# Performance work log

Measured on AMD Instinct MI355X. Metric: run time of the kernel, lower is better.

## Reference

```python
import jax, jax.numpy as jnp
import numpy as np

M, N = 1024, 4096


def setup_inputs() -> dict:
    key = jax.random.key(0)
    k1, k2, k3 = jax.random.split(key, 3)
    scores = jax.random.normal(k1, (M, N), dtype=jnp.float32)
    continuing_ag = jax.random.randint(k2, (M,), 0, 2).astype(jnp.int32)
    joint_action_prev = jax.random.randint(k3, (M,), 0, N).astype(jnp.int32)
    return {"scores": scores, "continuing_ag": continuing_ag,
            "joint_action_prev": joint_action_prev}


def _assign(policy, continuing_ag, joint_action_prev):
    """Sequential greedy bipartite assignment (train=False / argmax path)."""
    m, n = policy.shape
    cont = continuing_ag.astype(bool)
    # Pre-assign continuing agents and zero their rows and chosen columns.
    out0 = jnp.where(cont, joint_action_prev, jnp.full((m,), -1, jnp.int32))
    col_hit = (jnp.zeros((n,), jnp.float32)
               .at[joint_action_prev].add(continuing_ag.astype(jnp.float32))) > 0
    pol0 = policy * (~cont)[:, None].astype(policy.dtype) * (~col_hit)[None, :].astype(policy.dtype)
    rows = jnp.arange(m)
    cols = jnp.arange(n)

    def step(carry, i):
        pol, act = carry
        flat = pol.reshape(-1)
        idx = jnp.argmax(flat)
        # skip if this agent is continuing, or all entries already zeroed
        do = (~cont[i]) & jnp.any(flat > 0)
        a = idx // n
        t = (idx % n).astype(act.dtype)
        act = act.at[a].set(jnp.where(do, t, act[a]))
        keep = ~((rows == a)[:, None] | (cols == (idx % n))[None, :])
        pol = jnp.where(do, pol * keep.astype(pol.dtype), pol)
        return (pol, act), None

    (_, act), _ = jax.lax.scan(step, (pol0, out0), jnp.arange(m))
    return act


def reference(scores, continuing_ag, joint_action_prev):
    # get_policy: softmax over the flattened M*N score matrix
    policy = jax.nn.softmax(scores.reshape(-1)).reshape(scores.shape)
    actions = _assign(policy, continuing_ag, joint_action_prev)
    return actions, policy
```

## Files before the change

### kernel.cpp

```cpp
#include <hip/hip_runtime.h>
#include <cstdint>
#include <cstddef>

#define MROWS 1024
#define NCOLS 4096
#define KCAP 12

typedef unsigned long long u64;
typedef unsigned int u32;

__device__ inline u32 fkey(u32 b) { return (b & 0x80000000u) ? ~b : (b | 0x80000000u); }

__device__ inline int key_col(u64 k) { return (NCOLS - 1) - (int)(k & 0xFFFull); }
__device__ inline int key_row(u64 k) { return (MROWS - 1) - (int)((k >> 12) & 0x3FFull); }

#define WAVE_FENCE() __asm__ volatile("s_waitcnt lgkmcnt(0)" ::: "memory")

__device__ inline float wave_sum_f(float v) {
    #pragma unroll
    for (int off = 32; off >= 1; off >>= 1)
        v += __shfl_xor(v, off, 64);
    return v;
}
__device__ inline u64 wave_max_u64(u64 v) {
    #pragma unroll
    for (int off = 32; off >= 1; off >>= 1) {
        u64 o = __shfl_xor(v, off, 64);
        v = o > v ? o : v;
    }
    return v;
}
__device__ inline u64 umax64(u64 a, u64 b) { return a > b ? a : b; }

__global__ __launch_bounds__(256, 4) void k_prep(const float* __restrict__ s,
                                                 float* __restrict__ rowsum,
                                                 u64* __restrict__ keys_g) {
    __shared__ u64 list[4][KCAP];
    __shared__ u32 cnts[4];
    int w = threadIdx.x >> 6, lane = threadIdx.x & 63;
    int r = blockIdx.x * 4 + w;

    const float4* s4 = (const float4*)(s + (size_t)r * NCOLS);
    u64 rowpart = (u64)(MROWS - 1 - r) << 12;
    if (lane == 0) cnts[w] = 0u;
    WAVE_FENCE();

    float acc = 0.0f;
    #pragma unroll
    for (int j = 0; j < 16; ++j) {
        float4 v = s4[lane + j * 64];
        acc += __expf(v.x) + __expf(v.y) + __expf(v.z) + __expf(v.w);
        int c0 = 4 * (lane + j * 64);
        if (v.x > 2.85f) { u32 sl = atomicAdd(&cnts[w], 1u); if (sl < KCAP)
            list[w][sl] = ((u64)fkey(__float_as_uint(v.x)) << 22) | rowpart | (u64)(NCOLS - 1 - (c0 + 0)); }
        if (v.y > 2.85f) { u32 sl = atomicAdd(&cnts[w], 1u); if (sl < KCAP)
            list[w][sl] = ((u64)fkey(__float_as_uint(v.y)) << 22) | rowpart | (u64)(NCOLS - 1 - (c0 + 1)); }
        if (v.z > 2.85f) { u32 sl = atomicAdd(&cnts[w], 1u); if (sl < KCAP)
            list[w][sl] = ((u64)fkey(__float_as_uint(v.z)) << 22) | rowpart | (u64)(NCOLS - 1 - (c0 + 2)); }
        if (v.w > 2.85f) { u32 sl = atomicAdd(&cnts[w], 1u); if (sl < KCAP)
            list[w][sl] = ((u64)fkey(__float_as_uint(v.w)) << 22) | rowpart | (u64)(NCOLS - 1 - (c0 + 3)); }
    }
    acc = wave_sum_f(acc);
    if (lane == 0) rowsum[r] = acc;
    WAVE_FENCE();
    u32 n = cnts[w];

    for (int att = 1; att < 4; ++att) {
        if (n <= KCAP) break;
        float T = att == 1 ? 3.1f : att == 2 ? 3.4f : 3.8f;
        if (lane == 0) cnts[w] = 0u;
        WAVE_FENCE();
        #pragma unroll 4
        for (int j = 0; j < 16; ++j) {
            float4 v = s4[lane + j * 64];
            int c0 = 4 * (lane + j * 64);
            if (v.x > T) { u32 sl = atomicAdd(&cnts[w], 1u); if (sl < KCAP)
                list[w][sl] = ((u64)fkey(__float_as_uint(v.x)) << 22) | rowpart | (u64)(NCOLS - 1 - (c0 + 0)); }
            if (v.y > T) { u32 sl = atomicAdd(&cnts[w], 1u); if (sl < KCAP)
                list[w][sl] = ((u64)fkey(__float_as_uint(v.y)) << 22) | rowpart | (u64)(NCOLS - 1 - (c0 + 1)); }
            if (v.z > T) { u32 sl = atomicAdd(&cnts[w], 1u); if (sl < KCAP)
                list[w][sl] = ((u64)fkey(__float_as_uint(v.z)) << 22) | rowpart | (u64)(NCOLS - 1 - (c0 + 2)); }
            if (v.w > T) { u32 sl = atomicAdd(&cnts[w], 1u); if (sl < KCAP)
                list[w][sl] = ((u64)fkey(__float_as_uint(v.w)) << 22) | rowpart | (u64)(NCOLS - 1 - (c0 + 3)); }
        }
        WAVE_FENCE();
        n = cnts[w];
    }
    if (n > KCAP) n = 0;
    if (lane < KCAP)
        keys_g[(size_t)r * KCAP + lane] = (lane < n) ? list[w][lane] : 0ull;
}

__global__ __launch_bounds__(512, 1) void k_policy_match(const float* __restrict__ s,
                                                         const int* __restrict__ cont,
                                                         const int* __restrict__ prev,
                                                         const float* __restrict__ rowsum,
                                                         const u64* __restrict__ keys_g,
                                                         float* __restrict__ policy,
                                                         float* __restrict__ actions) {
    __shared__ u64 keybuf[MROWS * KCAP];
    __shared__ u64 colbest[NCOLS];
    __shared__ u64 cand[64];
    __shared__ u32 coldone[NCOLS / 32];
    __shared__ u32 rowdone[MROWS / 32];
    __shared__ float act[MROWS];
    __shared__ u32 leftrows[64];
    __shared__ int nleft;
    __shared__ float fredf[8];

    int t = threadIdx.x;
    int wid = t >> 6, lane = t & 63;

    if (blockIdx.x != 0) {
        int r = blockIdx.x - 1;
        const float4* srow4 = (const float4*)(s + (size_t)r * NCOLS);
        float4 v0 = srow4[t], v1 = srow4[t + 512];
        float sv = rowsum[t] + rowsum[t + 512];
        sv = wave_sum_f(sv);
        if (lane == 0) fredf[wid] = sv;
        __syncthreads();
        float g = 0.0f;
        #pragma unroll
        for (int i = 0; i < 8; ++i) g += fredf[i];
        float inv = 1.0f / g;
        float4* prow4 = (float4*)(policy + (size_t)r * NCOLS);
        float4 p;
        p.x = __expf(v0.x) * inv; p.y = __expf(v0.y) * inv;
        p.z = __expf(v0.z) * inv; p.w = __expf(v0.w) * inv;
        prow4[t] = p;
        p.x = __expf(v1.x) * inv; p.y = __expf(v1.y) * inv;
        p.z = __expf(v1.z) * inv; p.w = __expf(v1.w) * inv;
        prow4[t + 512] = p;
        return;
    }

    {
        const float4* kg4 = (const float4*)keys_g;
        float4* kb4 = (float4*)keybuf;
        #pragma unroll
        for (int i = 0; i < 12; ++i) kb4[t + i * 512] = kg4[t + i * 512];
        #pragma unroll
        for (int i = 0; i < 8; ++i) colbest[t + i * 512] = 0ull;
        if (t < 128) coldone[t] = 0u;
        if (t < 64) cand[t] = 0ull;
        if (t < 32) rowdone[t] = 0u;
        if (t == 0) nleft = 0;
    }
    __syncthreads();

    int r0 = t, r1 = t + 512;
    int c0f = cont[r0], c1f = cont[r1];
    int p0 = prev[r0], p1 = prev[r1];
    act[r0] = c0f ? (float)p0 : -1.0f;
    act[r1] = c1f ? (float)p1 : -1.0f;
    if (c0f) {
        atomicOr(&rowdone[r0 >> 5], 1u << (r0 & 31));
        atomicOr(&coldone[p0 >> 5], 1u << (p0 & 31));
    }
    if (c1f) {
        atomicOr(&rowdone[r1 >> 5], 1u << (r1 & 31));
        atomicOr(&coldone[p1 >> 5], 1u << (p1 & 31));
    }
    bool act0 = (c0f == 0), act1 = (c1f == 0);

    const u64* kb0 = keybuf + (size_t)r0 * KCAP;
    const u64* kb1 = keybuf + (size_t)r1 * KCAP;
    u32 m0 = 0u, m1 = 0u;
    #pragma unroll
    for (int k = 0; k < KCAP; ++k) {
        if (kb0[k] != 0ull) m0 |= 1u << k;
        if (kb1[k] != 0ull) m1 |= 1u << k;
    }
    if (m0 == 0u) act0 = false;
    if (m1 == 0u) act1 = false;
    __syncthreads();

    for (int round = 1; round < 500; ++round) {
        u64 tag = (u64)round << 54;
        bool sub0 = false, sub1 = false;
        u64 best0 = 0ull, best1 = 0ull;
        if (act0) {
            u32 m = m0;
            #pragma unroll
            for (int k = 0; k < KCAP; ++k) {
                if (m & (1u << k)) {
                    u64 kk = kb0[k];
                    int c = key_col(kk);
                    if ((coldone[c >> 5] >> (c & 31)) & 1u) m &= ~(1u << k);
                    else {
                        best0 = umax64(best0, kk);
                        atomicMax((u64*)&colbest[c], tag | kk);
                    }
                }
            }
            m0 = m;
            if (best0 == 0ull) act0 = false;
            else sub0 = true;
        }
        if (act1) {
            u32 m = m1;
            #pragma unroll
            for (int k = 0; k < KCAP; ++k) {
                if (m & (1u << k)) {
                    u64 kk = kb1[k];
                    int c = key_col(kk);
                    if ((coldone[c >> 5] >> (c & 31)) & 1u) m &= ~(1u << k);
                    else {
                        best1 = umax64(best1, kk);
                        atomicMax((u64*)&colbest[c], tag | kk);
                    }
                }
            }
            m1 = m;
            if (best1 == 0ull) act1 = false;
            else sub1 = true;
        }
        __syncthreads();
        if (sub0 && colbest[key_col(best0)] == (tag | best0)) {
            int c = key_col(best0);
            act[r0] = (float)c;
            atomicOr(&coldone[c >> 5], 1u << (c & 31));
            atomicOr(&rowdone[r0 >> 5], 1u << (r0 & 31));
            act0 = false;
        }
        if (sub1 && colbest[key_col(best1)] == (tag | best1)) {
            int c = key_col(best1);
            act[r1] = (float)c;
            atomicOr(&coldone[c >> 5], 1u << (c & 31));
            atomicOr(&rowdone[r1 >> 5], 1u << (r1 & 31));
            act1 = false;
        }
        int left = __syncthreads_count((act0 || act1) ? 1 : 0);
        if (left == 0) break;
    }
    __syncthreads();

    if (!((rowdone[r0 >> 5] >> (r0 & 31)) & 1u)) {
        int i = atomicAdd(&nleft, 1); if (i < 64) leftrows[i] = (u32)r0;
    }
    if (!((rowdone[r1 >> 5] >> (r1 & 31)) & 1u)) {
        int i = atomicAdd(&nleft, 1); if (i < 64) leftrows[i] = (u32)r1;
    }
    __syncthreads();
    int nl = nleft; if (nl > 64) nl = 64;
    if (nl > 0) {
        for (int i = 0; i < nl; ++i) {
            int rr = (int)leftrows[i];
            const float* srow = s + (size_t)rr * NCOLS;
            u64 rp = (u64)(MROWS - 1 - rr) << 12;
            u64 b = 0ull;
            #pragma unroll
            for (int j = 0; j < 8; ++j) {
                int c = t + j * 512;
                if (!((coldone[c >> 5] >> (c & 31)) & 1u))
                    b = umax64(b, ((u64)fkey(__float_as_uint(srow[c])) << 22) | rp |
                                  (u64)(NCOLS - 1 - c));
            }
            b = wave_max_u64(b);
            if (lane == 0 && b != 0ull) atomicMax((u64*)&cand[i], b);
        }
        __syncthreads();
        if (t < 64) {
            for (int guard = 0; guard < 96; ++guard) {
                for (int i = 0; i < nl; ++i) {
                    int rr = (int)leftrows[i];
                    if ((rowdone[rr >> 5] >> (rr & 31)) & 1u) continue;
                    u64 cd = cand[i];
                    int cc = key_col(cd);
                    if (cd != 0ull && !((coldone[cc >> 5] >> (cc & 31)) & 1u)) continue;
                    const float* srow = s + (size_t)rr * NCOLS;
                    u64 rp = (u64)(MROWS - 1 - rr) << 12;
                    u64 b = 0ull;
                    for (int c = lane; c < NCOLS; c += 64)
                        if (!((coldone[c >> 5] >> (c & 31)) & 1u))
                            b = umax64(b, ((u64)fkey(__float_as_uint(srow[c])) << 22) | rp |
                                          (u64)(NCOLS - 1 - c));
                    b = wave_max_u64(b);
                    if (lane == 0) cand[i] = b;
                    WAVE_FENCE();
                }
                u64 best = 0ull;
                for (int i = lane; i < nl; i += 64) {
                    int rr = (int)leftrows[i];
                    if (!((rowdone[rr >> 5] >> (rr & 31)) & 1u))
                        best = umax64(best, cand[i]);
                }
                best = wave_max_u64(best);
                if (best == 0ull) break;
                if (lane == 0) {
                    int row = key_row(best), col = key_col(best);
                    rowdone[row >> 5] |= 1u << (row & 31);
                    coldone[col >> 5] |= 1u << (col & 31);
                    act[row] = (float)col;
                }
                WAVE_FENCE();
            }
        }
    }
    __syncthreads();

    if (t < 64) {
        u32 miss = (t < 32) ? ~rowdone[t] : 0u;
        if (__ballot(miss != 0u) != 0ull) {
            for (int guard = 0; guard < 1200; ++guard) {
                u64 best = 0ull;
                for (int rr = 0; rr < MROWS; ++rr) {
                    if ((rowdone[rr >> 5] >> (rr & 31)) & 1u) continue;
                    const float* srow = s + (size_t)rr * NCOLS;
                    u64 rp = (u64)(MROWS - 1 - rr) << 12;
                    for (int c = t; c < NCOLS; c += 64) {
                        if ((coldone[c >> 5] >> (c & 31)) & 1u) continue;
                        u64 kk2 = ((u64)fkey(__float_as_uint(srow[c])) << 22) | rp |
                                  (u64)(NCOLS - 1 - c);
                        best = umax64(best, kk2);
                    }
                }
                best = wave_max_u64(best);
                if (best == 0ull) break;
                if (t == 0) {
                    int row = key_row(best), col = key_col(best);
                    rowdone[row >> 5] |= 1u << (row & 31);
                    coldone[col >> 5] |= 1u << (col & 31);
                    act[row] = (float)col;
                }
                WAVE_FENCE();
            }
        }
    }
    __syncthreads();
    actions[t] = act[t];
    actions[t + 512] = act[t + 512];
}

extern "C" void kernel_launch(void* const* d_in, const int* in_sizes, int n_in,
                              void* d_out, int out_size, void* d_ws, size_t ws_size,
                              hipStream_t stream) {
    (void)in_sizes; (void)n_in; (void)out_size; (void)ws_size;
    const float* scores = (const float*)d_in[0];
    const int* cont = (const int*)d_in[1];
    const int* prev = (const int*)d_in[2];
    float* out = (float*)d_out;
    float* actions = out;
    float* policy = out + MROWS;

    char* ws = (char*)d_ws;
    float* rowsum = (float*)(ws + 0);
    u64* keys12 = (u64*)(ws + 8192);

    k_prep<<<MROWS / 4, 256, 0, stream>>>(scores, rowsum, keys12);
    k_policy_match<<<MROWS + 1, 512, 0, stream>>>(scores, cont, prev, rowsum,
                                                  keys12, policy, actions);
}
```

Before: 101.5 us.

## Accumulate softmax total atomically and read match keys from global memory

k_prep now atomically adds each row's exp-sum into a single global total, which is zeroed by a memset. Each policy block then reads that one value instead of loading and reducing 1024 row sums with a block barrier. The matching block drops its 96 KB shared key buffer and its upfront copy, and reads keys straight from global (cached) memory in every round, treating zero keys as empty slots. This frees LDS and removes the startup copy and the barrier, at the cost of an extra memset launch, nondeterministic float summation order, and repeated global loads inside the serial matching loop.

```diff
diff --git a/kernel.cpp b/kernel.cpp
--- a/kernel.cpp
+++ b/kernel.cpp
@@ -33,7 +33,7 @@
 __device__ inline u64 umax64(u64 a, u64 b) { return a > b ? a : b; }
 
 __global__ __launch_bounds__(256, 4) void k_prep(const float* __restrict__ s,
-                                                 float* __restrict__ rowsum,
+                                                 float* __restrict__ total,
                                                  u64* __restrict__ keys_g) {
     __shared__ u64 list[4][KCAP];
     __shared__ u32 cnts[4];
@@ -61,7 +61,7 @@
             list[w][sl] = ((u64)fkey(__float_as_uint(v.w)) << 22) | rowpart | (u64)(NCOLS - 1 - (c0 + 3)); }
     }
     acc = wave_sum_f(acc);
-    if (lane == 0) rowsum[r] = acc;
+    if (lane == 0) atomicAdd(total, acc);
     WAVE_FENCE();
     u32 n = cnts[w];
 
@@ -94,11 +94,10 @@
 __global__ __launch_bounds__(512, 1) void k_policy_match(const float* __restrict__ s,
                                                          const int* __restrict__ cont,
                                                          const int* __restrict__ prev,
-                                                         const float* __restrict__ rowsum,
+                                                         const float* __restrict__ total,
                                                          const u64* __restrict__ keys_g,
                                                          float* __restrict__ policy,
                                                          float* __restrict__ actions) {
-    __shared__ u64 keybuf[MROWS * KCAP];
     __shared__ u64 colbest[NCOLS];
     __shared__ u64 cand[64];
     __shared__ u32 coldone[NCOLS / 32];
@@ -106,23 +105,15 @@
     __shared__ float act[MROWS];
     __shared__ u32 leftrows[64];
     __shared__ int nleft;
-    __shared__ float fredf[8];
 
     int t = threadIdx.x;
-    int wid = t >> 6, lane = t & 63;
+    int lane = t & 63;
 
     if (blockIdx.x != 0) {
         int r = blockIdx.x - 1;
         const float4* srow4 = (const float4*)(s + (size_t)r * NCOLS);
         float4 v0 = srow4[t], v1 = srow4[t + 512];
-        float sv = rowsum[t] + rowsum[t + 512];
-        sv = wave_sum_f(sv);
-        if (lane == 0) fredf[wid] = sv;
-        __syncthreads();
-        float g = 0.0f;
-        #pragma unroll
-        for (int i = 0; i < 8; ++i) g += fredf[i];
-        float inv = 1.0f / g;
+        float inv = 1.0f / *total;
         float4* prow4 = (float4*)(policy + (size_t)r * NCOLS);
         float4 p;
         p.x = __expf(v0.x) * inv; p.y = __expf(v0.y) * inv;
@@ -134,18 +125,12 @@
         return;
     }
 
-    {
-        const float4* kg4 = (const float4*)keys_g;
-        float4* kb4 = (float4*)keybuf;
-        #pragma unroll
-        for (int i = 0; i < 12; ++i) kb4[t + i * 512] = kg4[t + i * 512];
-        #pragma unroll
-        for (int i = 0; i < 8; ++i) colbest[t + i * 512] = 0ull;
-        if (t < 128) coldone[t] = 0u;
-        if (t < 64) cand[t] = 0ull;
-        if (t < 32) rowdone[t] = 0u;
-        if (t == 0) nleft = 0;
-    }
+    #pragma unroll
+    for (int i = 0; i < 8; ++i) colbest[t + i * 512] = 0ull;
+    if (t < 128) coldone[t] = 0u;
+    if (t < 64) cand[t] = 0ull;
+    if (t < 32) rowdone[t] = 0u;
+    if (t == 0) nleft = 0;
     __syncthreads();
 
     int r0 = t, r1 = t + 512;
@@ -163,16 +148,10 @@
     }
     bool act0 = (c0f == 0), act1 = (c1f == 0);
 
-    const u64* kb0 = keybuf + (size_t)r0 * KCAP;
-    const u64* kb1 = keybuf + (size_t)r1 * KCAP;
-    u32 m0 = 0u, m1 = 0u;
-    #pragma unroll
-    for (int k = 0; k < KCAP; ++k) {
-        if (kb0[k] != 0ull) m0 |= 1u << k;
-        if (kb1[k] != 0ull) m1 |= 1u << k;
-    }
-    if (m0 == 0u) act0 = false;
-    if (m1 == 0u) act1 = false;
+    const u64* kg0 = keys_g + (size_t)r0 * KCAP;
+    const u64* kg1 = keys_g + (size_t)r1 * KCAP;
+    u32 m0 = act0 ? 0xFFFu : 0u;
+    u32 m1 = act1 ? 0xFFFu : 0u;
     __syncthreads();
 
     for (int round = 1; round < 500; ++round) {
@@ -184,9 +163,10 @@
             #pragma unroll
             for (int k = 0; k < KCAP; ++k) {
                 if (m & (1u << k)) {
-                    u64 kk = kb0[k];
+                    u64 kk = kg0[k];
                     int c = key_col(kk);
-                    if ((coldone[c >> 5] >> (c & 31)) & 1u) m &= ~(1u << k);
+                    if (kk == 0ull || ((coldone[c >> 5] >> (c & 31)) & 1u))
+                        m &= ~(1u << k);
                     else {
                         best0 = umax64(best0, kk);
                         atomicMax((u64*)&colbest[c], tag | kk);
@@ -202,9 +182,10 @@
             #pragma unroll
             for (int k = 0; k < KCAP; ++k) {
                 if (m & (1u << k)) {
-                    u64 kk = kb1[k];
+                    u64 kk = kg1[k];
                     int c = key_col(kk);
-                    if ((coldone[c >> 5] >> (c & 31)) & 1u) m &= ~(1u << k);
+                    if (kk == 0ull || ((coldone[c >> 5] >> (c & 31)) & 1u))
+                        m &= ~(1u << k);
                     else {
                         best1 = umax64(best1, kk);
                         atomicMax((u64*)&colbest[c], tag | kk);
@@ -344,10 +325,11 @@
     float* policy = out + MROWS;
 
     char* ws = (char*)d_ws;
-    float* rowsum = (float*)(ws + 0);
+    float* total = (float*)(ws + 0);
     u64* keys12 = (u64*)(ws + 8192);
 
-    k_prep<<<MROWS / 4, 256, 0, stream>>>(scores, rowsum, keys12);
-    k_policy_match<<<MROWS + 1, 512, 0, stream>>>(scores, cont, prev, rowsum,
+    hipMemsetAsync(total, 0, 4, stream);
+    k_prep<<<MROWS / 4, 256, 0, stream>>>(scores, total, keys12);
+    k_policy_match<<<MROWS + 1, 512, 0, stream>>>(scores, cont, prev, total,
                                                   keys12, policy, actions);
 }
```

Result: slower. 121.2 us (+19.4%).
